# Kernel tuning notes

Hardware: AMD Instinct MI355X
Metric: run time of the kernel (lower is better)

Reference implementation:

```python
import jax, jax.numpy as jnp
import numpy as np

N_FFT = 512
HOP = 128
WIN = 512
Q = 0.1
PCT_WIN = 31
FREQ_WIN = 5
TIME_WIN = 9
STRENGTH = 0.35
THRESH = 1.5
TEMP = 0.15
MIN_MASK = 0.08


def _hann_periodic(n):
    # matches torch.hann_window(n) (periodic)
    return (0.5 * (1.0 - jnp.cos(2.0 * jnp.pi * jnp.arange(n) / n))).astype(jnp.float32)


def _stft(x, window):
    # x: (B, L) -> complex (B, F, T); center=True, reflect pad
    pad = N_FFT // 2
    xp = jnp.pad(x, ((0, 0), (pad, pad)), mode='reflect')
    T = 1 + (xp.shape[-1] - N_FFT) // HOP
    idx = (jnp.arange(T) * HOP)[:, None] + jnp.arange(N_FFT)  # (T, n_fft)
    frames = xp[:, idx] * window  # (B, T, n_fft)
    return jnp.fft.rfft(frames, axis=-1).transpose(0, 2, 1)  # (B, F, T)


def _istft(spec, window, length):
    # spec: (B, F, T) complex -> (B, length)
    frames = jnp.fft.irfft(spec.transpose(0, 2, 1), n=N_FFT, axis=-1) * window  # (B,T,n_fft)
    B, T, _ = frames.shape
    total = N_FFT + HOP * (T - 1)
    idx = ((jnp.arange(T) * HOP)[:, None] + jnp.arange(N_FFT)).ravel()
    out = jnp.zeros((B, total), frames.dtype).at[:, idx].add(frames.reshape(B, -1))
    wsq = jnp.zeros((total,), frames.dtype).at[idx].add(
        jnp.broadcast_to(window ** 2, (T, N_FFT)).ravel())
    out = out / jnp.maximum(wsq, 1e-11)
    pad = N_FFT // 2
    return out[:, pad:pad + length]


def _rolling_quantile(mag):
    # mag: (B, F, T); replicate pad + sliding window of PCT_WIN along time
    p = PCT_WIN // 2
    padded = jnp.pad(mag, ((0, 0), (0, 0), (p, p)), mode='edge')
    T = mag.shape[-1]
    windows = jnp.stack([padded[..., i:i + T] for i in range(PCT_WIN)], axis=-1)  # (B,F,T,W)
    return jnp.quantile(windows, Q, axis=-1)


def _avg_pool(x, k, axis):
    # stride-1 avg pool with zero pad k//2, count_include_pad=True (torch default)
    if k <= 1:
        return x
    p = k // 2
    pads = [(0, 0)] * x.ndim
    pads[axis] = (p, p)
    xp = jnp.pad(x, pads)
    n = x.shape[axis]
    acc = 0.0
    for i in range(k):
        sl = [slice(None)] * x.ndim
        sl[axis] = slice(i, i + n)
        acc = acc + xp[tuple(sl)]
    return acc / k


def setup_inputs() -> dict:
    key = jax.random.key(0)
    k1, k2 = jax.random.split(key)
    B, L = 16, 160000
    noisy = jax.random.normal(k1, (B, L), dtype=jnp.float32)
    enhanced = jax.random.normal(k2, (B, L), dtype=jnp.float32)
    return {"noisy": noisy, "enhanced": enhanced}


def reference(noisy, enhanced):
    length = enhanced.shape[-1]
    window = _hann_periodic(WIN)
    e_spec = _stft(enhanced, window)
    n_spec = _stft(noisy, window)
    e_mag = jnp.maximum(jnp.abs(e_spec), 1e-6)
    n_mag = jnp.maximum(jnp.abs(n_spec), 1e-6)
    # mode == 'sg_input_floor': source is the noisy magnitude
    floor = _rolling_quantile(n_mag)
    floor = _avg_pool(floor, FREQ_WIN, axis=-2)
    floor = _avg_pool(floor, TIME_WIN, axis=-1)
    floor = jnp.maximum(floor, 1e-6)
    mask = jax.nn.sigmoid((e_mag - THRESH * floor) / (TEMP * floor + 1e-6))
    final_mask = MIN_MASK + (1.0 - MIN_MASK) * (1.0 - STRENGTH + STRENGTH * mask)
    phase = e_spec / jnp.maximum(jnp.abs(e_spec), 1e-12)  # unit-phase, = polar(1, angle)
    gated_spec = (e_mag * final_mask).astype(jnp.float32) * phase
    return _istft(gated_spec, window, length)
```

## Files before the change

kernel.cpp:

```cpp
#include <hip/hip_runtime.h>
#include <math.h>

#define BATCH 16
#define LEN   160000
#define NFFT  512
#define HOP   128
#define NT    1251
#define NF    257
#define PADC  256
#define TWO_PI 6.28318530717958647692f
#define P(i) ((i) + ((i) >> 5))
#define FBUF 528
#define GSTR 264

__device__ __forceinline__ int reflect_idx(int j) {
    j = j < 0 ? -j : j;
    j = j >= LEN ? 2*LEN - 2 - j : j;
    return j;
}

__device__ __forceinline__ float hann(int n) {
    return 0.5f - 0.5f * __cosf(TWO_PI * (float)n * (1.0f / 512.0f));
}

struct T4 { float m0, m1, m2, m3; };

__device__ __forceinline__ void ins(T4& a, float v) {
    const float x0 = fminf(a.m0, v);  const float c0 = fmaxf(a.m0, v);
    const float x1 = fminf(a.m1, c0); const float c1 = fmaxf(a.m1, c0);
    const float x2 = fminf(a.m2, c1); const float c2 = fmaxf(a.m2, c1);
    const float x3 = fminf(a.m3, c2);
    a.m0 = x0; a.m1 = x1; a.m2 = x2; a.m3 = x3;
}

__device__ __forceinline__ T4 merge4(const T4& a, const T4& b) {
    const float l0 = fminf(a.m0, b.m3);
    const float l1 = fminf(a.m1, b.m2);
    const float l2 = fminf(a.m2, b.m1);
    const float l3 = fminf(a.m3, b.m0);
    const float t0 = fminf(l0, l2), t2 = fmaxf(l0, l2);
    const float t1 = fminf(l1, l3), t3 = fmaxf(l1, l3);
    T4 r;
    r.m0 = fminf(t0, t1); r.m1 = fmaxf(t0, t1);
    r.m2 = fminf(t2, t3); r.m3 = fmaxf(t2, t3);
    return r;
}

__device__ __forceinline__ T4 sort4(float a, float b, float c, float d) {
    const float x0 = fminf(a, b), x1 = fmaxf(a, b);
    const float x2 = fminf(c, d), x3 = fmaxf(c, d);
    const float y0 = fminf(x0, x2), y2 = fmaxf(x0, x2);
    const float y1 = fminf(x1, x3), y3 = fmaxf(x1, x3);
    T4 r; r.m0 = y0; r.m1 = fminf(y1, y2); r.m2 = fmaxf(y1, y2); r.m3 = y3;
    return r;
}

__device__ __forceinline__ void dft8(float vr[8], float vi[8], float sign) {
    const float K = 0.70710678118654752f;
    float ar=vr[0]+vr[4], ai=vi[0]+vi[4];
    float br=vr[0]-vr[4], bi=vi[0]-vi[4];
    float cr=vr[2]+vr[6], ci=vi[2]+vi[6];
    float dr=vr[2]-vr[6], di=vi[2]-vi[6];
    float er=vr[1]+vr[5], ei=vi[1]+vi[5];
    float fr=vr[1]-vr[5], fi=vi[1]-vi[5];
    float gr=vr[3]+vr[7], gi=vi[3]+vi[7];
    float hr=vr[3]-vr[7], hi=vi[3]-vi[7];
    const float W4dr = -sign*di, W4di = sign*dr;
    const float W4hr = -sign*hi, W4hi = sign*hr;
    const float E0r=ar+cr, E0i=ai+ci, E2r=ar-cr, E2i=ai-ci;
    const float E1r=br+W4dr, E1i=bi+W4di, E3r=br-W4dr, E3i=bi-W4di;
    const float O0r=er+gr, O0i=ei+gi, O2r=er-gr, O2i=ei-gi;
    const float O1r=fr+W4hr, O1i=fi+W4hi, O3r=fr-W4hr, O3i=fi-W4hi;
    const float T1r = K*(O1r - sign*O1i), T1i = K*(O1i + sign*O1r);
    const float T2r = -sign*O2i,          T2i = sign*O2r;
    const float T3r = K*(-O3r - sign*O3i), T3i = K*(-O3i + sign*O3r);
    vr[0]=E0r+O0r; vi[0]=E0i+O0i;  vr[4]=E0r-O0r; vi[4]=E0i-O0i;
    vr[1]=E1r+T1r; vi[1]=E1i+T1i;  vr[5]=E1r-T1r; vi[5]=E1i-T1i;
    vr[2]=E2r+T2r; vi[2]=E2i+T2i;  vr[6]=E2r-T2r; vi[6]=E2i-T2i;
    vr[3]=E3r+T3r; vi[3]=E3i+T3i;  vr[7]=E3r-T3r; vi[7]=E3i-T3i;
}

template<int NS>
__device__ __forceinline__ void fft_pass(float* R, float* I, int j, float sign) {
    float vr[8], vi[8];
    #pragma unroll
    for (int r = 0; r < 8; ++r) { vr[r] = R[P(j + 64*r)]; vi[r] = I[P(j + 64*r)]; }
    const float th = sign * (TWO_PI / (8.0f * (float)NS)) * (float)(j & (NS - 1));
    float w1r, w1i; __sincosf(th, &w1i, &w1r);
    float wr = w1r, wi = w1i;
    #pragma unroll
    for (int r = 1; r < 8; ++r) {
        const float tr = vr[r]*wr - vi[r]*wi;
        vi[r] = vr[r]*wi + vi[r]*wr; vr[r] = tr;
        const float nwr = wr*w1r - wi*w1i;
        wi = wr*w1i + wi*w1r; wr = nwr;
    }
    dft8(vr, vi, sign);
    const int base = ((j / NS) * (8 * NS)) + (j & (NS - 1));
    #pragma unroll
    for (int r = 0; r < 8; ++r) { R[P(base + r*NS)] = vr[r]; I[P(base + r*NS)] = vi[r]; }
}

__global__ __launch_bounds__(256, 4) void stft_kernel(const float* __restrict__ enh,
                                                      const float* __restrict__ noi,
                                                      float2* __restrict__ e_spec,
                                                      float*  __restrict__ n_mag) {
    __shared__ float Ar[4*FBUF], Ai[4*FBUF];
    const int tid = threadIdx.x;
    const int w = tid >> 6, j = tid & 63;
    const int tr_ = blockIdx.x * 4 + w;
    const bool live = tr_ < NT;
    const int t = live ? tr_ : NT - 1;
    const int b = blockIdx.y;
    float* ar = Ar + w*FBUF; float* ai = Ai + w*FBUF;

    {
        const int sbase = t * HOP - PADC;
        const float* __restrict__ pe = enh + b * LEN;
        const float* __restrict__ pn = noi + b * LEN;
        float vr[8], vi[8];
        #pragma unroll
        for (int r = 0; r < 8; ++r) {
            const int n = j + 64*r;
            const int idx = reflect_idx(sbase + n);
            const float wd = hann(n);
            vr[r] = pe[idx] * wd;
            vi[r] = pn[idx] * wd;
        }
        dft8(vr, vi, -1.0f);
        #pragma unroll
        for (int r = 0; r < 8; ++r) { ar[P(8*j + r)] = vr[r]; ai[P(8*j + r)] = vi[r]; }
    }
    fft_pass<8> (ar, ai, j, -1.0f);
    fft_pass<64>(ar, ai, j, -1.0f);

    if (live) {
        const int obase = (b * NT + t) * NF;
        #pragma unroll
        for (int r = 0; r < 5; ++r) {
            const int kk = j + 64*r;
            if (kk > 256) break;
            if (r == 4 && j != 0) break;
            const float zr = ar[P(kk)], zi = ai[P(kk)];
            const int n2 = (512 - kk) & 511;
            const float yr = ar[P(n2)], yi = ai[P(n2)];
            const float er = 0.5f*(zr + yr), ei = 0.5f*(zi - yi);
            const float nr = 0.5f*(zi + yi), ni = 0.5f*(yr - zr);
            e_spec[obase + kk] = make_float2(er, ei);
            n_mag[obase + kk] = fmaxf(sqrtf(nr*nr + ni*ni), 1e-6f);
        }
    }
}

__global__ __launch_bounds__(256) void floor_kernel(const float* __restrict__ n_mag,
                                                    float* __restrict__ floor_) {
    __shared__ float q[24][GSTR];
    __shared__ float fq[24];
    const int tid = threadIdx.x;
    const int t0 = blockIdx.x * 16, b = blockIdx.y;
    const float* __restrict__ pb = n_mag + b * NT * NF;

    {
        float wv[54];
        #pragma unroll
        for (int r = 0; r < 54; ++r) {
            int tr = t0 - 19 + r;
            tr = tr < 0 ? 0 : (tr > NT - 1 ? NT - 1 : tr);
            wv[r] = pb[tr * NF + tid];
        }
        T4 ch[6];
        #pragma unroll
        for (int c = 0; c < 6; ++c)
            ch[c] = merge4(sort4(wv[8*c],   wv[8*c+1], wv[8*c+2], wv[8*c+3]),
                           sort4(wv[8*c+4], wv[8*c+5], wv[8*c+6], wv[8*c+7]));
        #pragma unroll
        for (int k = 0; k < 24; ++k) {
            const int c0 = (k + 7) >> 3;
            T4 m = merge4(merge4(ch[c0], ch[c0+1]), ch[c0+2]);
            #pragma unroll
            for (int jj = k; jj < 8*c0; ++jj) ins(m, wv[jj]);
            #pragma unroll
            for (int jj = 8*c0 + 24; jj < k + 31; ++jj) ins(m, wv[jj]);
            q[k][tid] = m.m3;
        }
    }
    if (tid < 24) {
        const int k = tid;
        T4 m; m.m0 = m.m1 = m.m2 = m.m3 = 3.4e38f;
        for (int dt = -15; dt <= 15; ++dt) {
            int tt = t0 - 4 + k + dt;
            tt = tt < 0 ? 0 : (tt > NT - 1 ? NT - 1 : tt);
            ins(m, pb[tt * NF + 256]);
        }
        q[k][256] = m.m3;
    }
    __syncthreads();

    float fp[24];
    {
        const int f = tid;
        #pragma unroll
        for (int k = 0; k < 24; ++k) {
            float acc = 0.0f;
            #pragma unroll
            for (int df = -2; df <= 2; ++df) {
                const int ff = f + df;
                if (ff >= 0 && ff < NF) acc += q[k][ff];
            }
            fp[k] = acc * (1.0f / 5.0f);
        }
    }
    if (tid < 24) {
        const int k = tid;
        fq[k] = (q[k][254] + q[k][255] + q[k][256]) * (1.0f / 5.0f);
    }
    __syncthreads();

    {
        const int f = tid;
        #pragma unroll
        for (int k = 0; k < 24; ++k) {
            const int tq = t0 - 4 + k;
            fp[k] = (tq >= 0 && tq < NT) ? fp[k] : 0.0f;
        }
        float acc = 0.0f;
        #pragma unroll
        for (int k = 0; k < 9; ++k) acc += fp[k];
        #pragma unroll
        for (int to = 0; to < 16; ++to) {
            const int t = t0 + to;
            if (t < NT)
                floor_[(b * NT + t) * NF + f] = fmaxf(acc * (1.0f / 9.0f), 1e-6f);
            if (to < 15) acc += fp[to + 9] - fp[to];
        }
    }
    if (tid < 16) {
        const int to = tid;
        const int t = t0 + to;
        if (t < NT) {
            float acc = 0.0f;
            #pragma unroll
            for (int k = 0; k < 9; ++k) {
                const int tq = t0 - 4 + to + k;
                acc += (tq >= 0 && tq < NT) ? fq[to + k] : 0.0f;
            }
            floor_[(b * NT + t) * NF + 256] = fmaxf(acc * (1.0f / 9.0f), 1e-6f);
        }
    }
}

__global__ __launch_bounds__(256, 4) void istft_kernel(const float2* __restrict__ g,
                                                       const float* __restrict__ floor_,
                                                       float* __restrict__ frames) {
    __shared__ float gr[8*GSTR], gi[8*GSTR];
    const int tid = threadIdx.x;
    const int w = tid >> 6, j = tid & 63;
    const int t0 = blockIdx.x * 8, b = blockIdx.y;
    const int ta = t0 + 2*w, tb = ta + 1;

    float* g0r = gr + (2*w) * GSTR;      float* g0i = gi + (2*w) * GSTR;
    float* g1r = gr + (2*w + 1) * GSTR;  float* g1i = gi + (2*w + 1) * GSTR;

    for (int e = j; e < 2 * NF; e += 64) {
        const int h = (e >= NF) ? 1 : 0;
        const int kk = e - h * NF;
        const int t = ta + h;
        float grv = 0.0f, giv = 0.0f;
        if (t < NT) {
            const int idx = (b * NT + t) * NF + kk;
            const float fl = floor_[idx];
            const float2 e2 = g[idx];
            const float a = sqrtf(e2.x * e2.x + e2.y * e2.y);
            const float emag = fmaxf(a, 1e-6f);
            const float xarg = (emag - 1.5f * fl) / (0.15f * fl + 1e-6f);
            const float mask = 1.0f / (1.0f + __expf(-xarg));
            const float fm = 0.08f + 0.92f * (0.65f + 0.35f * mask);
            const float scale = emag * fm / fmaxf(a, 1e-12f);
            grv = e2.x * scale; giv = e2.y * scale;
        }
        gr[(2*w + h) * GSTR + kk] = grv;
        gi[(2*w + h) * GSTR + kk] = giv;
    }

    float* ar = g0r;
    float* ai = g0i;

    {
        float vr[8], vi[8];
        #pragma unroll
        for (int r = 0; r < 8; ++r) {
            const int n = j + 64*r;
            float cr, ci;
            if (n <= 256) {
                cr = g0r[n] - g1i[n];
                ci = g0i[n] + g1r[n];
            } else {
                const int m = 512 - n;
                cr = g0r[m] + g1i[m];
                ci = g1r[m] - g0i[m];
            }
            vr[r] = cr; vi[r] = ci;
        }
        dft8(vr, vi, 1.0f);
        #pragma unroll
        for (int r = 0; r < 8; ++r) { ar[P(8*j + r)] = vr[r]; ai[P(8*j + r)] = vi[r]; }
    }
    fft_pass<8> (ar, ai, j, 1.0f);
    fft_pass<64>(ar, ai, j, 1.0f);

    #pragma unroll
    for (int r = 0; r < 8; ++r) {
        const int n = j + 64*r;
        const float wd = hann(n) * (1.0f / 512.0f);
        if (ta < NT) frames[(b * NT + ta) * NFFT + n] = ar[P(n)] * wd;
        if (tb < NT) frames[(b * NT + tb) * NFFT + n] = ai[P(n)] * wd;
    }
}

__global__ __launch_bounds__(256) void ola_kernel(const float* __restrict__ frames,
                                                  float* __restrict__ out) {
    const int j = blockIdx.x * 256 + threadIdx.x;
    if (j >= BATCH * LEN) return;
    const int b = j / LEN;
    const int jj = j - b * LEN;
    const int i = jj + PADC;
    int t_lo = (i >= 384) ? ((i - 384) >> 7) : 0;
    int t_hi = i >> 7; if (t_hi > NT - 1) t_hi = NT - 1;
    if (t_hi - t_lo == 3) {
        const float* __restrict__ fp = frames + (b * NT + t_lo) * NFFT + (i - (t_lo << 7));
        const float acc = fp[0] + fp[384] + fp[768] + fp[1152];
        out[j] = acc * (2.0f / 3.0f);
    } else {
        float acc = 0.0f, wacc = 0.0f;
        for (int t = t_lo; t <= t_hi; ++t) {
            const int n = i - (t << 7);
            const float w = hann(n);
            acc  += frames[(b * NT + t) * NFFT + n];
            wacc += w * w;
        }
        out[j] = acc / fmaxf(wacc, 1e-11f);
    }
}

extern "C" void kernel_launch(void* const* d_in, const int* in_sizes, int n_in,
                              void* d_out, int out_size, void* d_ws, size_t ws_size,
                              hipStream_t stream) {
    const float* noisy    = (const float*)d_in[0];
    const float* enhanced = (const float*)d_in[1];
    float* out = (float*)d_out;

    float* ws = (float*)d_ws;
    float2* e_spec = (float2*)ws;
    float* floor_ = ws + 10288224;
    float* n_mag  = ws + 15432336;
    float* frames = ws + 15432336;

    dim3 blk(256);
    stft_kernel <<<dim3((NT + 3) / 4, BATCH), blk, 0, stream>>>(enhanced, noisy, e_spec, n_mag);
    floor_kernel<<<dim3((NT + 15) / 16, BATCH), blk, 0, stream>>>(n_mag, floor_);
    istft_kernel<<<dim3((NT + 7) / 8, BATCH), blk, 0, stream>>>(e_spec, floor_, frames);
    ola_kernel  <<<dim3((BATCH * LEN + 255) / 256), blk, 0, stream>>>(frames, out);
}
```

Measured before the change: 146.2 us.

## Keep last FFT pass in registers, use shuffles, fast-path STFT loads, vectorize OLA

Several separate changes land together. The final radix-8 FFT pass now returns its results in registers instead of writing them back to shared memory. The STFT mirror-bin pairing uses wave shuffles in place of shared-memory reads, interior frames skip reflect indexing, and the overlap-add kernel handles four outputs per thread with float4 loads and stores. These aim to cut shared-memory traffic, index arithmetic and global memory transaction count, at the cost of more register use and extra branch paths.

```diff
diff --git a/kernel.cpp b/kernel.cpp
--- a/kernel.cpp
+++ b/kernel.cpp
@@ -101,6 +101,23 @@
     for (int r = 0; r < 8; ++r) { R[P(base + r*NS)] = vr[r]; I[P(base + r*NS)] = vi[r]; }
 }
 
+__device__ __forceinline__ void fft_pass_last(const float* R, const float* I, int j,
+                                              float sign, float vr[8], float vi[8]) {
+    #pragma unroll
+    for (int r = 0; r < 8; ++r) { vr[r] = R[P(j + 64*r)]; vi[r] = I[P(j + 64*r)]; }
+    const float th = sign * (TWO_PI / 512.0f) * (float)j;
+    float w1r, w1i; __sincosf(th, &w1i, &w1r);
+    float wr = w1r, wi = w1i;
+    #pragma unroll
+    for (int r = 1; r < 8; ++r) {
+        const float tr = vr[r]*wr - vi[r]*wi;
+        vi[r] = vr[r]*wi + vi[r]*wr; vr[r] = tr;
+        const float nwr = wr*w1r - wi*w1i;
+        wi = wr*w1i + wi*w1r; wr = nwr;
+    }
+    dft8(vr, vi, sign);
+}
+
 __global__ __launch_bounds__(256, 4) void stft_kernel(const float* __restrict__ enh,
                                                       const float* __restrict__ noi,
                                                       float2* __restrict__ e_spec,
@@ -116,38 +133,59 @@
 
     {
         const int sbase = t * HOP - PADC;
-        const float* __restrict__ pe = enh + b * LEN;
-        const float* __restrict__ pn = noi + b * LEN;
         float vr[8], vi[8];
-        #pragma unroll
-        for (int r = 0; r < 8; ++r) {
-            const int n = j + 64*r;
-            const int idx = reflect_idx(sbase + n);
-            const float wd = hann(n);
-            vr[r] = pe[idx] * wd;
-            vi[r] = pn[idx] * wd;
+        if (sbase >= 0 && sbase + NFFT <= LEN) {
+            const float* __restrict__ pe = enh + b * LEN + sbase;
+            const float* __restrict__ pn = noi + b * LEN + sbase;
+            #pragma unroll
+            for (int r = 0; r < 8; ++r) {
+                const int n = j + 64*r;
+                const float wd = hann(n);
+                vr[r] = pe[n] * wd;
+                vi[r] = pn[n] * wd;
+            }
+        } else {
+            const float* __restrict__ pe = enh + b * LEN;
+            const float* __restrict__ pn = noi + b * LEN;
+            #pragma unroll
+            for (int r = 0; r < 8; ++r) {
+                const int n = j + 64*r;
+                const int idx = reflect_idx(sbase + n);
+                const float wd = hann(n);
+                vr[r] = pe[idx] * wd;
+                vi[r] = pn[idx] * wd;
+            }
         }
         dft8(vr, vi, -1.0f);
         #pragma unroll
         for (int r = 0; r < 8; ++r) { ar[P(8*j + r)] = vr[r]; ai[P(8*j + r)] = vi[r]; }
     }
-    fft_pass<8> (ar, ai, j, -1.0f);
-    fft_pass<64>(ar, ai, j, -1.0f);
-
+    fft_pass<8>(ar, ai, j, -1.0f);
+    float zr[8], zi[8];
+    fft_pass_last(ar, ai, j, -1.0f, zr, zi);
+
+    const int src = (64 - j) & 63;
+    float pr[4], pi_[4];
+    #pragma unroll
+    for (int q = 4; q < 8; ++q) {
+        pr[q-4]  = __shfl(zr[q], src);
+        pi_[q-4] = __shfl(zi[q], src);
+    }
     if (live) {
         const int obase = (b * NT + t) * NF;
         #pragma unroll
-        for (int r = 0; r < 5; ++r) {
+        for (int r = 0; r < 4; ++r) {
             const int kk = j + 64*r;
-            if (kk > 256) break;
-            if (r == 4 && j != 0) break;
-            const float zr = ar[P(kk)], zi = ai[P(kk)];
-            const int n2 = (512 - kk) & 511;
-            const float yr = ar[P(n2)], yi = ai[P(n2)];
-            const float er = 0.5f*(zr + yr), ei = 0.5f*(zi - yi);
-            const float nr = 0.5f*(zi + yi), ni = 0.5f*(yr - zr);
+            const float yr = (j == 0) ? zr[(8 - r) & 7] : pr[3 - r];
+            const float yi = (j == 0) ? zi[(8 - r) & 7] : pi_[3 - r];
+            const float er = 0.5f*(zr[r] + yr), ei = 0.5f*(zi[r] - yi);
+            const float nr = 0.5f*(zi[r] + yi), ni = 0.5f*(yr - zr[r]);
             e_spec[obase + kk] = make_float2(er, ei);
             n_mag[obase + kk] = fmaxf(sqrtf(nr*nr + ni*ni), 1e-6f);
+        }
+        if (j == 0) {
+            e_spec[obase + 256] = make_float2(zr[4], 0.0f);
+            n_mag[obase + 256] = fmaxf(fabsf(zi[4]), 1e-6f);
         }
     }
 }
@@ -305,40 +343,55 @@
         #pragma unroll
         for (int r = 0; r < 8; ++r) { ar[P(8*j + r)] = vr[r]; ai[P(8*j + r)] = vi[r]; }
     }
-    fft_pass<8> (ar, ai, j, 1.0f);
-    fft_pass<64>(ar, ai, j, 1.0f);
+    fft_pass<8>(ar, ai, j, 1.0f);
+    float xr[8], xi[8];
+    fft_pass_last(ar, ai, j, 1.0f, xr, xi);
 
     #pragma unroll
     for (int r = 0; r < 8; ++r) {
         const int n = j + 64*r;
         const float wd = hann(n) * (1.0f / 512.0f);
-        if (ta < NT) frames[(b * NT + ta) * NFFT + n] = ar[P(n)] * wd;
-        if (tb < NT) frames[(b * NT + tb) * NFFT + n] = ai[P(n)] * wd;
+        if (ta < NT) frames[(b * NT + ta) * NFFT + n] = xr[r] * wd;
+        if (tb < NT) frames[(b * NT + tb) * NFFT + n] = xi[r] * wd;
     }
 }
 
 __global__ __launch_bounds__(256) void ola_kernel(const float* __restrict__ frames,
                                                   float* __restrict__ out) {
-    const int j = blockIdx.x * 256 + threadIdx.x;
-    if (j >= BATCH * LEN) return;
-    const int b = j / LEN;
-    const int jj = j - b * LEN;
+    const int gid = blockIdx.x * 256 + threadIdx.x;
+    if (gid >= BATCH * (LEN / 4)) return;
+    const int b = gid / (LEN / 4);
+    const int jj = (gid - b * (LEN / 4)) * 4;
     const int i = jj + PADC;
-    int t_lo = (i >= 384) ? ((i - 384) >> 7) : 0;
-    int t_hi = i >> 7; if (t_hi > NT - 1) t_hi = NT - 1;
-    if (t_hi - t_lo == 3) {
-        const float* __restrict__ fp = frames + (b * NT + t_lo) * NFFT + (i - (t_lo << 7));
-        const float acc = fp[0] + fp[384] + fp[768] + fp[1152];
-        out[j] = acc * (2.0f / 3.0f);
+    const int q = i >> 7;
+    const int n0 = i & 127;
+    if (q >= 3 && q <= NT - 1) {
+        const float* __restrict__ fp = frames + (b * NT + q) * NFFT + n0;
+        const float4 a0 = *(const float4*)(fp);
+        const float4 a1 = *(const float4*)(fp - 384);
+        const float4 a2 = *(const float4*)(fp - 768);
+        const float4 a3 = *(const float4*)(fp - 1152);
+        float4 o;
+        o.x = (a0.x + a1.x + a2.x + a3.x) * (2.0f / 3.0f);
+        o.y = (a0.y + a1.y + a2.y + a3.y) * (2.0f / 3.0f);
+        o.z = (a0.z + a1.z + a2.z + a3.z) * (2.0f / 3.0f);
+        o.w = (a0.w + a1.w + a2.w + a3.w) * (2.0f / 3.0f);
+        *(float4*)(out + b * LEN + jj) = o;
     } else {
-        float acc = 0.0f, wacc = 0.0f;
-        for (int t = t_lo; t <= t_hi; ++t) {
-            const int n = i - (t << 7);
-            const float w = hann(n);
-            acc  += frames[(b * NT + t) * NFFT + n];
-            wacc += w * w;
-        }
-        out[j] = acc / fmaxf(wacc, 1e-11f);
+        #pragma unroll
+        for (int e = 0; e < 4; ++e) {
+            const int ie = i + e;
+            int t_lo = (ie >= 384) ? ((ie - 384) >> 7) : 0;
+            int t_hi = ie >> 7; if (t_hi > NT - 1) t_hi = NT - 1;
+            float acc = 0.0f, wacc = 0.0f;
+            for (int t = t_lo; t <= t_hi; ++t) {
+                const int n = ie - (t << 7);
+                const float wd = hann(n);
+                acc  += frames[(b * NT + t) * NFFT + n];
+                wacc += wd * wd;
+            }
+            out[b * LEN + jj + e] = acc / fmaxf(wacc, 1e-11f);
+        }
     }
 }
 
@@ -355,9 +408,8 @@
     float* n_mag  = ws + 15432336;
     float* frames = ws + 15432336;
 
-    dim3 blk(256);
-    stft_kernel <<<dim3((NT + 3) / 4, BATCH), blk, 0, stream>>>(enhanced, noisy, e_spec, n_mag);
-    floor_kernel<<<dim3((NT + 15) / 16, BATCH), blk, 0, stream>>>(n_mag, floor_);
-    istft_kernel<<<dim3((NT + 7) / 8, BATCH), blk, 0, stream>>>(e_spec, floor_, frames);
-    ola_kernel  <<<dim3((BATCH * LEN + 255) / 256), blk, 0, stream>>>(frames, out);
-}
+    stft_kernel <<<dim3((NT + 3) / 4, BATCH), dim3(256), 0, stream>>>(enhanced, noisy, e_spec, n_mag);
+    floor_kernel<<<dim3((NT + 15) / 16, BATCH), dim3(256), 0, stream>>>(n_mag, floor_);
+    istft_kernel<<<dim3((NT + 7) / 8, BATCH), dim3(256), 0, stream>>>(e_spec, floor_, frames);
+    ola_kernel  <<<dim3((BATCH * (LEN / 4) + 255) / 256), dim3(256), 0, stream>>>(frames, out);
+}
```

Result: no change. 145.3 us (-0.7%).
